# Kernel tuning notes

Hardware: AMD Instinct MI355X
Metric: run time of the kernel (lower is better)

The kernel has to match this reference:

```python
import jax, jax.numpy as jnp
import numpy as np

N, D, H, W = 2, 16, 32, 32
C, G, K = 64, 4, 3
PAD, STRIDE, DIL = 1, 1, 1
OS = 1.0
GC = C // G
P = K * K * K
EPS = 1e-6


def setup_inputs() -> dict:
    key = jax.random.key(0)
    ks = jax.random.split(key, 8)
    s = 1.0 / np.sqrt(C)
    return {
        "input": jax.random.normal(ks[0], (N, D, H, W, C), jnp.float32),
        "dw_w": jax.random.normal(ks[1], (C, 1, K, K, K), jnp.float32) * 0.05,
        "dw_b": jnp.zeros((C,), jnp.float32),
        "ln_g": jnp.ones((C,), jnp.float32),
        "ln_b": jnp.zeros((C,), jnp.float32),
        "off_w": jax.random.normal(ks[2], (G * P * 3, C), jnp.float32) * 0.02,
        "off_b": jax.random.normal(ks[3], (G * P * 3,), jnp.float32) * 0.1,
        "mask_w": jax.random.normal(ks[4], (G * P, C), jnp.float32) * 0.02,
        "mask_b": jnp.zeros((G * P,), jnp.float32),
        "in_w": jax.random.normal(ks[5], (C, C), jnp.float32) * s,
        "in_b": jnp.zeros((C,), jnp.float32),
        "out_w": jax.random.normal(ks[6], (C, C), jnp.float32) * s,
        "out_b": jnp.zeros((C,), jnp.float32),
    }


def _grid_sample_3d(inp, grid):
    # inp: (B, Cc, Dd, Hh, Ww); grid: (B, L, Pp, 3) with (x, y, z) in [-1, 1]
    # trilinear, padding_mode='zeros', align_corners=False (torch F.grid_sample semantics)
    B, Cc, Dd, Hh, Ww = inp.shape
    L, Pp = grid.shape[1], grid.shape[2]
    px = ((grid[..., 0] + 1.0) * Ww - 1.0) * 0.5
    py = ((grid[..., 1] + 1.0) * Hh - 1.0) * 0.5
    pz = ((grid[..., 2] + 1.0) * Dd - 1.0) * 0.5
    x0 = jnp.floor(px).astype(jnp.int32)
    y0 = jnp.floor(py).astype(jnp.int32)
    z0 = jnp.floor(pz).astype(jnp.int32)
    fx = px - x0
    fy = py - y0
    fz = pz - z0
    flat = inp.reshape(B, Cc, Dd * Hh * Ww)

    def gather(zi, yi, xi, wt):
        valid = (xi >= 0) & (xi < Ww) & (yi >= 0) & (yi < Hh) & (zi >= 0) & (zi < Dd)
        idx = (jnp.clip(zi, 0, Dd - 1) * Hh + jnp.clip(yi, 0, Hh - 1)) * Ww + jnp.clip(xi, 0, Ww - 1)
        g = jax.vmap(lambda f, i: f[:, i])(flat, idx.reshape(B, -1))  # (B, Cc, L*Pp)
        w = (wt * valid.astype(wt.dtype)).reshape(B, 1, -1)
        return g * w

    out = gather(z0, y0, x0, (1 - fz) * (1 - fy) * (1 - fx))
    out = out + gather(z0, y0, x0 + 1, (1 - fz) * (1 - fy) * fx)
    out = out + gather(z0, y0 + 1, x0, (1 - fz) * fy * (1 - fx))
    out = out + gather(z0, y0 + 1, x0 + 1, (1 - fz) * fy * fx)
    out = out + gather(z0 + 1, y0, x0, fz * (1 - fy) * (1 - fx))
    out = out + gather(z0 + 1, y0, x0 + 1, fz * (1 - fy) * fx)
    out = out + gather(z0 + 1, y0 + 1, x0, fz * fy * (1 - fx))
    out = out + gather(z0 + 1, y0 + 1, x0 + 1, fz * fy * fx)
    return out.reshape(B, Cc, L, Pp)


def _forward(input, dw_w, dw_b, ln_g, ln_b, off_w, off_b, mask_w, mask_b, in_w, in_b, out_w, out_b):
    N_, D_, H_, W_, C_ = input.shape
    # input projection (value path)
    x = input @ in_w.T + in_b
    # depthwise conv -> LayerNorm (channels_last) -> GELU  (the x1 / query path)
    xc = jnp.transpose(input, (0, 4, 1, 2, 3))
    pad = (DIL * 0 + (K - 1)) // 2  # dw_kernel_size == kernel_size, 'same' padding
    y = jax.lax.conv_general_dilated(
        xc, dw_w, window_strides=(1, 1, 1), padding=[(pad, pad)] * 3,
        dimension_numbers=("NCDHW", "OIDHW", "NCDHW"), feature_group_count=C_)
    y = y + dw_b[None, :, None, None, None]
    x1 = jnp.transpose(y, (0, 2, 3, 4, 1))
    mu = x1.mean(-1, keepdims=True)
    var = x1.var(-1, keepdims=True)
    x1 = (x1 - mu) * jax.lax.rsqrt(var + EPS) * ln_g + ln_b
    x1 = jax.nn.gelu(x1, approximate=False)
    # offset and mask heads
    offset = x1 @ off_w.T + off_b                       # (N, D, H, W, G*P*3)
    mlog = (x1 @ mask_w.T + mask_b).reshape(N_, D_, H_, W_, G, P)
    mask = jax.nn.softmax(mlog, axis=-1).reshape(N_, D_, H_, W_, G * P)
    # ---- dcnv3 core ----
    xp = jnp.pad(x, ((0, 0), (PAD, PAD), (PAD, PAD), (PAD, PAD), (0, 0)))
    Din, Hin, Win = D_ + 2 * PAD, H_ + 2 * PAD, W_ + 2 * PAD
    Dout = (Din - (DIL * (K - 1) + 1)) // STRIDE + 1
    Hout = (Hin - (DIL * (K - 1) + 1)) // STRIDE + 1
    Wout = (Win - (DIL * (K - 1) + 1)) // STRIDE + 1
    base = DIL * (K - 1) // 2 + 0.5
    rz = (base + jnp.arange(Dout, dtype=jnp.float32) * STRIDE) / Din
    ry = (base + jnp.arange(Hout, dtype=jnp.float32) * STRIDE) / Hin
    rx = (base + jnp.arange(Wout, dtype=jnp.float32) * STRIDE) / Win
    Z, Y, X = jnp.meshgrid(rz, ry, rx, indexing="ij")
    ref = jnp.stack([X, Y, Z], -1)                       # (Dout, Hout, Wout, 3) in (x,y,z)
    # dilation kernel grid; torch iterates (kw, kh, kd) with 'ij' meshgrid
    off1 = jnp.arange(K, dtype=jnp.float32) * DIL - (DIL * (K - 1) // 2)
    gx, gy, gz = jnp.meshgrid(off1 / Win, off1 / Hin, off1 / Din, indexing="ij")
    gridk = jnp.stack([gx, gy, gz], -1).reshape(P, 3)    # (P, 3), same for every group
    loc = ref[None, :, :, :, None, None, :] + OS * gridk[None, None, None, None, None, :, :]
    offs = offset.reshape(N_, Dout, Hout, Wout, G, P, 3)
    norm = jnp.array([Win, Hin, Din], jnp.float32)
    loc = loc + offs * OS / norm                         # (N, Dout, Hout, Wout, G, P, 3)
    sg = 2.0 * loc - 1.0
    L = Dout * Hout * Wout
    x_ = xp.reshape(N_, Din, Hin, Win, G, GC)
    x_ = jnp.transpose(x_, (0, 4, 5, 1, 2, 3)).reshape(N_ * G, GC, Din, Hin, Win)
    grid_ = sg.reshape(N_, L, G, P, 3)
    grid_ = jnp.transpose(grid_, (0, 2, 1, 3, 4)).reshape(N_ * G, L, P, 3)
    samp = _grid_sample_3d(x_, grid_)                    # (N*G, GC, L, P)
    m_ = jnp.transpose(mask.reshape(N_, L, G, P), (0, 2, 1, 3)).reshape(N_ * G, 1, L, P)
    out = (samp * m_).sum(-1)                            # (N*G, GC, L)
    out = jnp.transpose(out.reshape(N_, G * GC, L), (0, 2, 1)).reshape(N_, Dout, Hout, Wout, C_)
    return out @ out_w.T + out_b


def reference(input, dw_w, dw_b, ln_g, ln_b, off_w, off_b, mask_w, mask_b, in_w, in_b, out_w, out_b):
    return _forward(input, dw_w, dw_b, ln_g, ln_b, off_w, off_b, mask_w, mask_b, in_w, in_b, out_w, out_b)
```

## Files before the change

### kernel.cpp

```cpp
#include <hip/hip_runtime.h>
#include <math.h>

#define NN 2
#define DD 16
#define HH 32
#define WW 32
#define DIN 18
#define HIN 34
#define WIN 34
#define NVOX 32768
#define NPAD (NN*DIN*HIN*WIN)
#define PLANE (DIN*HIN*WIN)
#define ROWS 432
#define SOMSTR 436

#define WS_XPG     16
#define XPG_FLOATS (NPAD*32)
#define WS_DWT     (WS_XPG + XPG_FLOATS + 16)
#define WS_CMBB    (WS_DWT + 1728)
#define WS_OUTB    (WS_CMBB + 13824)

#define PREP_DWT   1728
#define PREP_CMB   27648
#define PREP_OUT   4096
#define PREP_PADS  32
#define PREP_TOTAL (PREP_DWT + PREP_CMB + PREP_OUT + PREP_PADS)
#define PREP_BLOCKS 131

typedef short  bf16x8 __attribute__((ext_vector_type(8)));
typedef float  f32x4  __attribute__((ext_vector_type(4)));

__device__ __forceinline__ unsigned short f2bf(float x) {
    unsigned u = __builtin_bit_cast(unsigned, x);
    u += 0x7fff + ((u >> 16) & 1);
    return (unsigned short)(u >> 16);
}
__device__ __forceinline__ float bf2f(unsigned short v) {
    return __builtin_bit_cast(float, ((unsigned)v) << 16);
}
__device__ __forceinline__ float bflo(unsigned u) {
    return __builtin_bit_cast(float, u << 16);
}
__device__ __forceinline__ float bfhi(unsigned u) {
    return __builtin_bit_cast(float, u & 0xffff0000u);
}
__device__ __forceinline__ bf16x8 pack8(float4 a, float4 b) {
    bf16x8 r;
    r[0] = (short)f2bf(a.x); r[1] = (short)f2bf(a.y);
    r[2] = (short)f2bf(a.z); r[3] = (short)f2bf(a.w);
    r[4] = (short)f2bf(b.x); r[5] = (short)f2bf(b.y);
    r[6] = (short)f2bf(b.z); r[7] = (short)f2bf(b.w);
    return r;
}

__global__ __launch_bounds__(256) void prep_vp(
        const float* __restrict__ inp,
        const float* __restrict__ in_w,  const float* __restrict__ out_w,
        const float* __restrict__ off_w, const float* __restrict__ mask_w,
        const float* __restrict__ dw_w,  const float* __restrict__ in_b,
        float* __restrict__ ws) {
    __shared__ __align__(16) unsigned short inB[4096];

    int t = threadIdx.x;
    int b = blockIdx.x;

    for (int i = t; i < 4096; i += 256) inB[i] = f2bf(in_w[i]);

    if (b < PREP_BLOCKS) {
        int idx = b * 256 + t;
        if (idx < PREP_DWT) {
            int k = idx >> 6, c = idx & 63;
            ws[WS_DWT + idx] = dw_w[c * 27 + k];
        } else if (idx < PREP_DWT + PREP_CMB) {
            int j = idx - PREP_DWT;
            ((unsigned short*)(ws + WS_CMBB))[j] =
                f2bf(j < 20736 ? off_w[j] : mask_w[j - 20736]);
        } else if (idx < PREP_DWT + PREP_CMB + PREP_OUT) {
            int j = idx - PREP_DWT - PREP_CMB;
            ((unsigned short*)(ws + WS_OUTB))[j] = f2bf(out_w[j]);
        } else if (idx < PREP_TOTAL) {
            int j = idx - PREP_DWT - PREP_CMB - PREP_OUT;
            if (j < 16) ws[j] = 0.f;
            else        ws[WS_XPG + XPG_FLOATS + (j - 16)] = 0.f;
        }
    }
    __syncthreads();

    unsigned short* xpg = (unsigned short*)(ws + WS_XPG);
    int lane = t & 63;
    int nid = lane & 15, quad = lane >> 4;

    int pv = b * 16 + nid;
    int wp = pv % 34, hp = (pv / 34) % 34, dp = (pv / 1156) % 18, n = pv / 20808;
    bool interior = (wp >= 1 && wp <= 32 && hp >= 1 && hp <= 32 && dp >= 1 && dp <= 16);

    bf16x8 b0 = {0,0,0,0,0,0,0,0}, b1 = {0,0,0,0,0,0,0,0};
    if (interior) {
        int vox = (((n * 16 + (dp - 1)) * 32 + (hp - 1)) * 32) + (wp - 1);
        const float* ip = inp + (size_t)vox * 64;
        b0 = pack8(*(const float4*)(ip + quad * 8),
                   *(const float4*)(ip + quad * 8 + 4));
        b1 = pack8(*(const float4*)(ip + quad * 8 + 32),
                   *(const float4*)(ip + quad * 8 + 36));
    }

    #pragma unroll
    for (int tt = 0; tt < 4; ++tt) {
        bf16x8 a0 = *(const bf16x8*)&inB[(16 * tt + nid) * 64 + quad * 8];
        bf16x8 a1 = *(const bf16x8*)&inB[(16 * tt + nid) * 64 + quad * 8 + 32];
        f32x4 acc = {0.f, 0.f, 0.f, 0.f};
        acc = __builtin_amdgcn_mfma_f32_16x16x32_bf16(a0, b0, acc, 0, 0, 0);
        acc = __builtin_amdgcn_mfma_f32_16x16x32_bf16(a1, b1, acc, 0, 0, 0);
        float bs0 = in_b[16 * tt + 4 * quad + 0];
        float bs1 = in_b[16 * tt + 4 * quad + 1];
        float bs2 = in_b[16 * tt + 4 * quad + 2];
        float bs3 = in_b[16 * tt + 4 * quad + 3];
        unsigned d0 = 0u, d1 = 0u;
        if (interior) {
            d0 = (unsigned)f2bf(acc[0] + bs0) | ((unsigned)f2bf(acc[1] + bs1) << 16);
            d1 = (unsigned)f2bf(acc[2] + bs2) | ((unsigned)f2bf(acc[3] + bs3) << 16);
        }
        *(uint2*)&xpg[((size_t)tt * NPAD + pv) * 16 + 4 * quad] = make_uint2(d0, d1);
    }
}

__global__ __launch_bounds__(256, 6) void dcn_main(
        const float* __restrict__ inp,
        const float* __restrict__ dw_b,
        const float* __restrict__ ln_g,  const float* __restrict__ ln_b,
        const float* __restrict__ off_b, const float* __restrict__ mask_b,
        const float* __restrict__ ws_ro,
        const float* __restrict__ out_b,
        float* __restrict__ out) {
    const unsigned short* xpg  = (const unsigned short*)(ws_ro + WS_XPG);
    const float* dwT  = ws_ro + WS_DWT;
    const unsigned short* cmbB = (const unsigned short*)(ws_ro + WS_CMBB);
    const unsigned short* outB = (const unsigned short*)(ws_ro + WS_OUTB);

    __shared__ __align__(16) unsigned short s_a[16 * 64];
    __shared__ __align__(16) unsigned short s_om2[16 * SOMSTR];
    __shared__ __align__(16) unsigned short s_vb[16 * 64];

    int t = threadIdx.x;
    int u = t >> 6, lane = t & 63;
    int nid = lane & 15, quad = lane >> 4;
    int hw = blockIdx.x;
    int L = (hw & 7) * 256 + (hw >> 3);
    int vox0 = L * 16;
    int w0 = vox0 & 31;
    int h0 = (vox0 >> 5) & 31;
    int d0 = (vox0 >> 10) & 15;
    int n  = vox0 >> 14;

    {
        int c = lane;
        float dwb = dw_b[c];
        float acc[4] = {dwb, dwb, dwb, dwb};
        int wbase = w0 + u * 4;
        #pragma unroll
        for (int kd = 0; kd < 3; ++kd) {
            int dz = d0 + kd - 1;
            if ((unsigned)dz >= DD) continue;
            #pragma unroll
            for (int kh = 0; kh < 3; ++kh) {
                int hy = h0 + kh - 1;
                if ((unsigned)hy >= HH) continue;
                const float* rowp = inp + ((((size_t)n * DD + dz) * HH + hy) * WW) * 64 + c;
                float cv[6];
                #pragma unroll
                for (int j = 0; j < 6; ++j) {
                    int wx = wbase - 1 + j;
                    cv[j] = ((unsigned)wx < WW) ? rowp[(size_t)wx * 64] : 0.f;
                }
                float wt0 = dwT[(kd * 9 + kh * 3 + 0) * 64 + c];
                float wt1 = dwT[(kd * 9 + kh * 3 + 1) * 64 + c];
                float wt2 = dwT[(kd * 9 + kh * 3 + 2) * 64 + c];
                #pragma unroll
                for (int i = 0; i < 4; ++i) {
                    acc[i] = fmaf(cv[i],     wt0, acc[i]);
                    acc[i] = fmaf(cv[i + 1], wt1, acc[i]);
                    acc[i] = fmaf(cv[i + 2], wt2, acc[i]);
                }
            }
        }
        #pragma unroll
        for (int i = 0; i < 4; ++i) {
            float a = acc[i];
            float s = a, ss = a * a;
            #pragma unroll
            for (int m = 1; m < 64; m <<= 1) {
                s  += __shfl_xor(s,  m, 64);
                ss += __shfl_xor(ss, m, 64);
            }
            float mu  = s * (1.f / 64.f);
            float var = ss * (1.f / 64.f) - mu * mu;
            float x1 = (a - mu) * rsqrtf(var + 1e-6f) * ln_g[c] + ln_b[c];
            x1 = 0.5f * x1 * (1.f + erff(x1 * 0.70710678118654752f));
            s_a[(u * 4 + i) * 64 + c] = f2bf(x1);
        }
    }
    __syncthreads();

    {
        bf16x8 a0 = *(const bf16x8*)&s_a[nid * 64 + quad * 8];
        bf16x8 a1 = *(const bf16x8*)&s_a[nid * 64 + quad * 8 + 32];
        for (int tl = u; tl < 27; tl += 4) {
            int r = tl * 16 + nid;
            bf16x8 b0 = *(const bf16x8*)&cmbB[r * 64 + quad * 8];
            bf16x8 b1 = *(const bf16x8*)&cmbB[r * 64 + quad * 8 + 32];
            f32x4 acc = {0.f, 0.f, 0.f, 0.f};
            acc = __builtin_amdgcn_mfma_f32_16x16x32_bf16(a0, b0, acc, 0, 0, 0);
            acc = __builtin_amdgcn_mfma_f32_16x16x32_bf16(a1, b1, acc, 0, 0, 0);
            float bias;
            int addr;
            if (r < 324) {
                bias = off_b[r];
                addr = (r / 3) * 4 + (r % 3);
            } else {
                bias = mask_b[r - 324];
                addr = (r - 324) * 4 + 3;
            }
            #pragma unroll
            for (int k = 0; k < 4; ++k)
                s_om2[(quad * 4 + k) * SOMSTR + addr] = f2bf(acc[k] + bias);
        }
    }
    __syncthreads();

    {
        int pair = t >> 2, l = t & 3;
        int vb = pair >> 2, g = pair & 3;
        unsigned short* m = &s_om2[vb * SOMSTR + g * 108];
        float e[7];
        float mx = -1e30f;
        #pragma unroll
        for (int j = 0; j < 7; ++j) {
            int p = l + 4 * j;
            float v = (p < 27) ? bf2f(m[p * 4 + 3]) : -1e30f;
            e[j] = v;
            mx = fmaxf(mx, v);
        }
        mx = fmaxf(mx, __shfl_xor(mx, 1, 64));
        mx = fmaxf(mx, __shfl_xor(mx, 2, 64));
        float sm = 0.f;
        #pragma unroll
        for (int j = 0; j < 7; ++j) {
            int p = l + 4 * j;
            e[j] = (p < 27) ? expf(e[j] - mx) : 0.f;
            sm += e[j];
        }
        sm += __shfl_xor(sm, 1, 64);
        sm += __shfl_xor(sm, 2, 64);
        float inv = 1.f / sm;
        #pragma unroll
        for (int j = 0; j < 7; ++j) {
            int p = l + 4 * j;
            if (p < 27) m[p * 4 + 3] = f2bf(e[j] * inv);
        }
    }
    __syncthreads();

    {
        int vb = lane >> 2, q = lane & 3;
        int chalf = q & 1, xhalf = q >> 1;
        int qo = q * 8;
        int wv = w0 + vb;
        const unsigned short* omb = &s_om2[vb * SOMSTR + u * 108];
        const unsigned short* xg = xpg + ((size_t)u * NPAD + (size_t)n * PLANE) * 16;
        float acc[8] = {0.f, 0.f, 0.f, 0.f, 0.f, 0.f, 0.f, 0.f};
        int p = 0;
        #pragma unroll
        for (int ix = 0; ix < 3; ++ix)
        #pragma unroll
        for (int iy = 0; iy < 3; ++iy)
        #pragma unroll
        for (int iz = 0; iz < 3; ++iz, ++p) {
            uint2 om4 = *(const uint2*)&omb[p * 4];
            float ox = bflo(om4.x), oy = bfhi(om4.x);
            float oz = bflo(om4.y), msk = bfhi(om4.y);
            float px = (float)(wv + ix) + ox;
            float py = (float)(h0 + iy) + oy;
            float pz = (float)(d0 + iz) + oz;
            float fx0 = floorf(px); int x0 = (int)fx0; float fx = px - fx0;
            float fy0 = floorf(py); int y0 = (int)fy0; float fy = py - fy0;
            float fz0 = floorf(pz); int z0 = (int)fz0; float fz = pz - fz0;
            float wx0 = ((unsigned)x0       < WIN) ? (1.f - fx) : 0.f;
            float wx1 = ((unsigned)(x0 + 1) < WIN) ? fx         : 0.f;
            float wy0 = ((unsigned)y0       < HIN) ? (1.f - fy) : 0.f;
            float wy1 = ((unsigned)(y0 + 1) < HIN) ? fy         : 0.f;
            float wz0 = ((unsigned)z0       < DIN) ? (1.f - fz) : 0.f;
            float wz1 = ((unsigned)(z0 + 1) < DIN) ? fz         : 0.f;
            wz0 *= msk; wz1 *= msk;
            int x0c = min(max(x0, -1), WIN - 1);
            int y0c = min(max(y0, 0), HIN - 1), y1c = min(max(y0 + 1, 0), HIN - 1);
            int z0c = min(max(z0, 0), DIN - 1), z1c = min(max(z0 + 1, 0), DIN - 1);
            int zb0 = z0c * (HIN * WIN), zb1 = z1c * (HIN * WIN);
            int yb0 = y0c * WIN,         yb1 = y1c * WIN;
            int r00 = zb0 + yb0 + x0c;
            int r01 = zb0 + yb1 + x0c;
            int r10 = zb1 + yb0 + x0c;
            int r11 = zb1 + yb1 + x0c;
            uint4 t00 = *(const uint4*)(xg + r00 * 16 + qo);
            uint4 t01 = *(const uint4*)(xg + r01 * 16 + qo);
            uint4 t10 = *(const uint4*)(xg + r10 * 16 + qo);
            uint4 t11 = *(const uint4*)(xg + r11 * 16 + qo);
            float wxq = xhalf ? wx1 : wx0;
            float w00 = wxq * wz0 * wy0;
            float w01 = wxq * wz0 * wy1;
            float w10 = wxq * wz1 * wy0;
            float w11 = wxq * wz1 * wy1;
            #define ACC8(T, W) { float w_ = (W); \
                acc[0] = fmaf(w_, bflo(T.x), acc[0]); acc[1] = fmaf(w_, bfhi(T.x), acc[1]); \
                acc[2] = fmaf(w_, bflo(T.y), acc[2]); acc[3] = fmaf(w_, bfhi(T.y), acc[3]); \
                acc[4] = fmaf(w_, bflo(T.z), acc[4]); acc[5] = fmaf(w_, bfhi(T.z), acc[5]); \
                acc[6] = fmaf(w_, bflo(T.w), acc[6]); acc[7] = fmaf(w_, bfhi(T.w), acc[7]); }
            ACC8(t00, w00) ACC8(t01, w01) ACC8(t10, w10) ACC8(t11, w11)
            #undef ACC8
        }
        #pragma unroll
        for (int i = 0; i < 8; ++i) acc[i] += __shfl_xor(acc[i], 2, 64);
        if (q < 2) {
            unsigned d0 = (unsigned)f2bf(acc[0]) | ((unsigned)f2bf(acc[1]) << 16);
            unsigned d1 = (unsigned)f2bf(acc[2]) | ((unsigned)f2bf(acc[3]) << 16);
            unsigned d2 = (unsigned)f2bf(acc[4]) | ((unsigned)f2bf(acc[5]) << 16);
            unsigned d3 = (unsigned)f2bf(acc[6]) | ((unsigned)f2bf(acc[7]) << 16);
            *(uint4*)&s_vb[vb * 64 + u * 16 + chalf * 8] = make_uint4(d0, d1, d2, d3);
        }
    }
    __syncthreads();

    {
        bf16x8 a0 = *(const bf16x8*)&s_vb[nid * 64 + quad * 8];
        bf16x8 a1 = *(const bf16x8*)&s_vb[nid * 64 + quad * 8 + 32];
        bf16x8 b0 = *(const bf16x8*)&outB[(u * 16 + nid) * 64 + quad * 8];
        bf16x8 b1 = *(const bf16x8*)&outB[(u * 16 + nid) * 64 + quad * 8 + 32];
        f32x4 acc = {0.f, 0.f, 0.f, 0.f};
        acc = __builtin_amdgcn_mfma_f32_16x16x32_bf16(a0, b0, acc, 0, 0, 0);
        acc = __builtin_amdgcn_mfma_f32_16x16x32_bf16(a1, b1, acc, 0, 0, 0);
        float ob = out_b[u * 16 + nid];
        #pragma unroll
        for (int k = 0; k < 4; ++k)
            out[(size_t)(vox0 + quad * 4 + k) * 64 + u * 16 + nid] = acc[k] + ob;
    }
}

extern "C" void kernel_launch(void* const* d_in, const int* in_sizes, int n_in,
                              void* d_out, int out_size, void* d_ws, size_t ws_size,
                              hipStream_t stream) {
    const float* inp    = (const float*)d_in[0];
    const float* dw_w   = (const float*)d_in[1];
    const float* dw_b   = (const float*)d_in[2];
    const float* ln_g   = (const float*)d_in[3];
    const float* ln_b   = (const float*)d_in[4];
    const float* off_w  = (const float*)d_in[5];
    const float* off_b  = (const float*)d_in[6];
    const float* mask_w = (const float*)d_in[7];
    const float* mask_b = (const float*)d_in[8];
    const float* in_w   = (const float*)d_in[9];
    const float* in_b   = (const float*)d_in[10];
    const float* out_w  = (const float*)d_in[11];
    const float* out_b  = (const float*)d_in[12];

    float* ws = (float*)d_ws;

    prep_vp<<<NPAD / 16, 256, 0, stream>>>(inp, in_w, out_w, off_w, mask_w,
                                           dw_w, in_b, ws);
    dcn_main<<<NVOX / 16, 256, 0, stream>>>(inp, dw_b, ln_g, ln_b,
                                            off_b, mask_b, ws, out_b,
                                            (float*)d_out);
}
```

Baseline: 158.4 us.

## Share sampling coordinate math across lane quads via shuffles; widen prep blocks

In the deformable sampling loop, each of the four lanes serving a voxel now computes the trilinear indices and weights for a different kernel point. The results are broadcast with shuffles, so the floor, clamp and weight arithmetic is no longer repeated four times. The prep kernel also now uses all four wavefronts per block, with 64 padded voxels per block and a bounds guard, instead of one 16-voxel slice per block. The change adds ten shuffles per sample point and a ragged tail for the 27th point.

```diff
diff --git a/kernel.cpp b/kernel.cpp
--- a/kernel.cpp
+++ b/kernel.cpp
@@ -26,6 +26,7 @@
 #define PREP_PADS  32
 #define PREP_TOTAL (PREP_DWT + PREP_CMB + PREP_OUT + PREP_PADS)
 #define PREP_BLOCKS 131
+#define VP_BLOCKS  651
 
 typedef short  bf16x8 __attribute__((ext_vector_type(8)));
 typedef float  f32x4  __attribute__((ext_vector_type(4)));
@@ -87,12 +88,14 @@
     __syncthreads();
 
     unsigned short* xpg = (unsigned short*)(ws + WS_XPG);
-    int lane = t & 63;
+    int u = t >> 6, lane = t & 63;
     int nid = lane & 15, quad = lane >> 4;
 
-    int pv = b * 16 + nid;
+    int pv = b * 64 + u * 16 + nid;
+    bool in_range = pv < NPAD;
     int wp = pv % 34, hp = (pv / 34) % 34, dp = (pv / 1156) % 18, n = pv / 20808;
-    bool interior = (wp >= 1 && wp <= 32 && hp >= 1 && hp <= 32 && dp >= 1 && dp <= 16);
+    bool interior = in_range &&
+        (wp >= 1 && wp <= 32 && hp >= 1 && hp <= 32 && dp >= 1 && dp <= 16);
 
     bf16x8 b0 = {0,0,0,0,0,0,0,0}, b1 = {0,0,0,0,0,0,0,0};
     if (interior) {
@@ -120,7 +123,8 @@
             d0 = (unsigned)f2bf(acc[0] + bs0) | ((unsigned)f2bf(acc[1] + bs1) << 16);
             d1 = (unsigned)f2bf(acc[2] + bs2) | ((unsigned)f2bf(acc[3] + bs3) << 16);
         }
-        *(uint2*)&xpg[((size_t)tt * NPAD + pv) * 16 + 4 * quad] = make_uint2(d0, d1);
+        if (in_range)
+            *(uint2*)&xpg[((size_t)tt * NPAD + pv) * 16 + 4 * quad] = make_uint2(d0, d1);
     }
 }
 
@@ -264,20 +268,19 @@
         int vb = lane >> 2, q = lane & 3;
         int chalf = q & 1, xhalf = q >> 1;
         int qo = q * 8;
+        int qbase = lane & 0x3C;
         int wv = w0 + vb;
         const unsigned short* omb = &s_om2[vb * SOMSTR + u * 108];
         const unsigned short* xg = xpg + ((size_t)u * NPAD + (size_t)n * PLANE) * 16;
         float acc[8] = {0.f, 0.f, 0.f, 0.f, 0.f, 0.f, 0.f, 0.f};
-        int p = 0;
-        #pragma unroll
-        for (int ix = 0; ix < 3; ++ix)
-        #pragma unroll
-        for (int iy = 0; iy < 3; ++iy)
-        #pragma unroll
-        for (int iz = 0; iz < 3; ++iz, ++p) {
-            uint2 om4 = *(const uint2*)&omb[p * 4];
+        #pragma unroll
+        for (int c = 0; c < 7; ++c) {
+            int pown = 4 * c + q;
+            int pc = pown < 27 ? pown : 26;
+            uint2 om4 = *(const uint2*)&omb[pc * 4];
             float ox = bflo(om4.x), oy = bfhi(om4.x);
             float oz = bflo(om4.y), msk = bfhi(om4.y);
+            int ix = pc / 9, r9 = pc - ix * 9, iy = r9 / 3, iz = r9 - iy * 3;
             float px = (float)(wv + ix) + ox;
             float py = (float)(h0 + iy) + oy;
             float pz = (float)(d0 + iz) + oz;
@@ -296,26 +299,39 @@
             int z0c = min(max(z0, 0), DIN - 1), z1c = min(max(z0 + 1, 0), DIN - 1);
             int zb0 = z0c * (HIN * WIN), zb1 = z1c * (HIN * WIN);
             int yb0 = y0c * WIN,         yb1 = y1c * WIN;
-            int r00 = zb0 + yb0 + x0c;
-            int r01 = zb0 + yb1 + x0c;
-            int r10 = zb1 + yb0 + x0c;
-            int r11 = zb1 + yb1 + x0c;
-            uint4 t00 = *(const uint4*)(xg + r00 * 16 + qo);
-            uint4 t01 = *(const uint4*)(xg + r01 * 16 + qo);
-            uint4 t10 = *(const uint4*)(xg + r10 * 16 + qo);
-            uint4 t11 = *(const uint4*)(xg + r11 * 16 + qo);
-            float wxq = xhalf ? wx1 : wx0;
-            float w00 = wxq * wz0 * wy0;
-            float w01 = wxq * wz0 * wy1;
-            float w10 = wxq * wz1 * wy0;
-            float w11 = wxq * wz1 * wy1;
-            #define ACC8(T, W) { float w_ = (W); \
-                acc[0] = fmaf(w_, bflo(T.x), acc[0]); acc[1] = fmaf(w_, bfhi(T.x), acc[1]); \
-                acc[2] = fmaf(w_, bflo(T.y), acc[2]); acc[3] = fmaf(w_, bfhi(T.y), acc[3]); \
-                acc[4] = fmaf(w_, bflo(T.z), acc[4]); acc[5] = fmaf(w_, bfhi(T.z), acc[5]); \
-                acc[6] = fmaf(w_, bflo(T.w), acc[6]); acc[7] = fmaf(w_, bfhi(T.w), acc[7]); }
-            ACC8(t00, w00) ACC8(t01, w01) ACC8(t10, w10) ACC8(t11, w11)
-            #undef ACC8
+            int sr00 = zb0 + yb0 + x0c, sr01 = zb0 + yb1 + x0c;
+            int sr10 = zb1 + yb0 + x0c, sr11 = zb1 + yb1 + x0c;
+            float sm00 = wz0 * wy0, sm01 = wz0 * wy1;
+            float sm10 = wz1 * wy0, sm11 = wz1 * wy1;
+            #pragma unroll
+            for (int j = 0; j < 4; ++j) {
+                if (4 * c + j >= 27) break;
+                int src = qbase + j;
+                int a00 = __shfl(sr00, src, 64);
+                int a01 = __shfl(sr01, src, 64);
+                int a10 = __shfl(sr10, src, 64);
+                int a11 = __shfl(sr11, src, 64);
+                float b00 = __shfl(sm00, src, 64);
+                float b01 = __shfl(sm01, src, 64);
+                float b10 = __shfl(sm10, src, 64);
+                float b11 = __shfl(sm11, src, 64);
+                float x0w = __shfl(wx0, src, 64);
+                float x1w = __shfl(wx1, src, 64);
+                uint4 t00 = *(const uint4*)(xg + a00 * 16 + qo);
+                uint4 t01 = *(const uint4*)(xg + a01 * 16 + qo);
+                uint4 t10 = *(const uint4*)(xg + a10 * 16 + qo);
+                uint4 t11 = *(const uint4*)(xg + a11 * 16 + qo);
+                float wxq = xhalf ? x1w : x0w;
+                float w00 = wxq * b00, w01 = wxq * b01;
+                float w10 = wxq * b10, w11 = wxq * b11;
+                #define ACC8(T, W) { float w_ = (W); \
+                    acc[0] = fmaf(w_, bflo(T.x), acc[0]); acc[1] = fmaf(w_, bfhi(T.x), acc[1]); \
+                    acc[2] = fmaf(w_, bflo(T.y), acc[2]); acc[3] = fmaf(w_, bfhi(T.y), acc[3]); \
+                    acc[4] = fmaf(w_, bflo(T.z), acc[4]); acc[5] = fmaf(w_, bfhi(T.z), acc[5]); \
+                    acc[6] = fmaf(w_, bflo(T.w), acc[6]); acc[7] = fmaf(w_, bfhi(T.w), acc[7]); }
+                ACC8(t00, w00) ACC8(t01, w01) ACC8(t10, w10) ACC8(t11, w11)
+                #undef ACC8
+            }
         }
         #pragma unroll
         for (int i = 0; i < 8; ++i) acc[i] += __shfl_xor(acc[i], 2, 64);
@@ -363,7 +379,7 @@
 
     float* ws = (float*)d_ws;
 
-    prep_vp<<<NPAD / 16, 256, 0, stream>>>(inp, in_w, out_w, off_w, mask_w,
+    prep_vp<<<VP_BLOCKS, 256, 0, stream>>>(inp, in_w, out_w, off_w, mask_w,
                                            dw_w, in_b, ws);
     dcn_main<<<NVOX / 16, 256, 0, stream>>>(inp, dw_b, ln_g, ln_b,
                                             off_b, mask_b, ws, out_b,
```

Result: slower. 262.7 us (+65.8%).
